# Performance work log

Measured on AMD Instinct MI355X. Metric: run time of the kernel, lower is better.

## Reference

```python
import jax, jax.numpy as jnp
import numpy as np

NUM_CODEBOOKS = 2
CODEBOOK_SIZE = 256
OUT_GROUP = 1
IN_GROUP = 8
IN_FEATURES = 4096
OUT_FEATURES = 11008


def setup_inputs() -> dict:
    key = jax.random.key(0)
    k1, k2, k3, k4, k5 = jax.random.split(key, 5)
    num_out_groups = OUT_FEATURES // OUT_GROUP
    num_in_groups = IN_FEATURES // IN_GROUP
    x = jax.random.normal(k1, (4, 2048, IN_FEATURES), dtype=jnp.float32)
    codes = jax.random.randint(k2, (num_out_groups, num_in_groups, NUM_CODEBOOKS), 0, CODEBOOK_SIZE, dtype=jnp.int32)
    codebooks = jax.random.normal(k3, (NUM_CODEBOOKS, CODEBOOK_SIZE, OUT_GROUP, IN_GROUP), dtype=jnp.float32) * 0.05
    scales = jax.random.uniform(k4, (num_out_groups, 1, 1, 1), dtype=jnp.float32)
    bias = jax.random.normal(k5, (OUT_FEATURES,), dtype=jnp.float32)
    return {"x": x, "codes": codes, "codebooks": codebooks, "scales": scales, "bias": bias}


def _dequantize_weight(codes, codebooks, scales):
    # codes: [Og, Ig, C] int; codebooks: [C, K, og, ig]; scales: [Og,1,1,1]
    C = codebooks.shape[0]
    og, ig = codebooks.shape[2], codebooks.shape[3]
    Og, Ig = codes.shape[0], codes.shape[1]
    # gather per-codebook vectors: result [Og, Ig, C, og, ig]
    w = codebooks[jnp.arange(C)[None, None, :], codes]
    w = w.sum(axis=2)                      # [Og, Ig, og, ig] (additive quantization)
    w = w * scales                         # broadcast [Og,1,1,1]
    w = w.transpose(0, 2, 1, 3)            # [Og, og, Ig, ig]
    return w.reshape(Og * og, Ig * ig)     # [out_features, in_features]


def reference(x, codes, codebooks, scales, bias):
    W = _dequantize_weight(codes, codebooks, scales)
    return jnp.einsum('bsi,oi->bso', x, W) + bias
```

## Files before the change

### kernel.cpp

```cpp
#include <hip/hip_runtime.h>
#include <hip/hip_bf16.h>
#include <stdint.h>

#define IN_F 4096
#define OUT_F 11008
#define M_ROWS 8192
#define NIG 512
#define CBSZ 256

typedef _Float16 f16x8 __attribute__((ext_vector_type(8)));
typedef float f32x4 __attribute__((ext_vector_type(4)));

__global__ __launch_bounds__(256) void dequant_w_kernel(
    const int* __restrict__ codes, const float* __restrict__ cbs,
    _Float16* __restrict__ W)
{
  const int idx = blockIdx.x * 256 + threadIdx.x;
  const int2 c = ((const int2*)codes)[idx];
  const float4* e0 = (const float4*)(cbs + (size_t)c.x * 8);
  const float4* e1 = (const float4*)(cbs + (size_t)CBSZ * 8 + (size_t)c.y * 8);
  const float4 a0 = e0[0], a1 = e0[1];
  const float4 b0 = e1[0], b1 = e1[1];
  f16x8 w;
  w[0] = (_Float16)(a0.x + b0.x);
  w[1] = (_Float16)(a0.y + b0.y);
  w[2] = (_Float16)(a0.z + b0.z);
  w[3] = (_Float16)(a0.w + b0.w);
  w[4] = (_Float16)(a1.x + b1.x);
  w[5] = (_Float16)(a1.y + b1.y);
  w[6] = (_Float16)(a1.z + b1.z);
  w[7] = (_Float16)(a1.w + b1.w);
  *(f16x8*)(W + (size_t)idx * 8) = w;
}

__global__ __launch_bounds__(256) void convert_x_kernel(
    const float* __restrict__ x, _Float16* __restrict__ X)
{
  const size_t i = ((size_t)blockIdx.x * 256 + threadIdx.x) * 8;
  const float4 a = *(const float4*)(x + i);
  const float4 b = *(const float4*)(x + i + 4);
  f16x8 v;
  v[0] = (_Float16)a.x; v[1] = (_Float16)a.y;
  v[2] = (_Float16)a.z; v[3] = (_Float16)a.w;
  v[4] = (_Float16)b.x; v[5] = (_Float16)b.y;
  v[6] = (_Float16)b.z; v[7] = (_Float16)b.w;
  *(f16x8*)(X + i) = v;
}

#define BM 256
#define BN 256
#define BK 64
#define NKT (IN_F / BK)
#define GRID_MT (M_ROWS / BM)
#define GRID_NT (OUT_F / BN)

__global__ __launch_bounds__(512, 2) void gemm_pipe(
    const _Float16* __restrict__ X, const _Float16* __restrict__ Wd,
    const float* __restrict__ scales, const float* __restrict__ bias,
    float* __restrict__ out)
{
  __shared__ char smem[131072];

  const int cpx = (GRID_MT * GRID_NT) >> 3;
  const int wg = (blockIdx.x & 7) * cpx + (blockIdx.x >> 3);
  const int mt = wg & (GRID_MT - 1), nt = wg >> 5;
  const int m0 = mt * BM, n0 = nt * BN;

  const int t = threadIdx.x;
  const int wave = t >> 6, lane = t & 63;
  const int wm = wave >> 2, wn = wave & 3;
  const int r16 = lane & 15;
  const int q = lane >> 4;
  const int sw = r16 & 7;
  const int c0 = ((q ^ sw) << 4);
  const int c1 = (((4 | q) ^ sw) << 4);

  const int s_row0 = t >> 3;
  const int s_col  = (((t & 7) ^ ((t >> 3) & 7)) << 3);
  const _Float16* asrc = X  + (size_t)(m0 + s_row0) * IN_F + s_col;
  const _Float16* bsrc = Wd + (size_t)(n0 + s_row0) * IN_F + s_col;
  const int s_dst = wave * 1024;

  f32x4 acc[8][4] = {};
  f16x8 alo[4][2], ahi[4][2], blo[2][2], bhi[2][2];

#define STAGE(kt, b) do {                                                     \
    const _Float16* _a = asrc + (size_t)(kt) * BK;                            \
    const _Float16* _b = bsrc + (size_t)(kt) * BK;                            \
    _Pragma("unroll")                                                         \
    for (int i = 0; i < 4; ++i)                                               \
      __builtin_amdgcn_global_load_lds(                                       \
        (const __attribute__((address_space(1))) void*)(_a + (size_t)i * 64 * IN_F), \
        (__attribute__((address_space(3))) void*)(smem + (b) * 65536 + i * 8192 + s_dst), \
        16, 0, 0);                                                            \
    _Pragma("unroll")                                                         \
    for (int i = 0; i < 4; ++i)                                               \
      __builtin_amdgcn_global_load_lds(                                       \
        (const __attribute__((address_space(1))) void*)(_b + (size_t)i * 64 * IN_F), \
        (__attribute__((address_space(3))) void*)(smem + (b) * 65536 + 32768 + i * 8192 + s_dst), \
        16, 0, 0);                                                            \
  } while (0)

#define BAR   __builtin_amdgcn_s_barrier()
#define PRIO1 __builtin_amdgcn_s_setprio(1)
#define PRIO0 __builtin_amdgcn_s_setprio(0)
#define VMCNT8 asm volatile("s_waitcnt vmcnt(8)" ::: "memory")
#define VMCNT0 asm volatile("s_waitcnt vmcnt(0)" ::: "memory")

#define QUAD(AM, BM_, AOFF, BOFF)                                             \
    _Pragma("unroll")                                                         \
    for (int k = 0; k < 2; ++k)                                               \
      _Pragma("unroll")                                                       \
      for (int m = 0; m < 4; ++m)                                             \
        _Pragma("unroll")                                                     \
        for (int n = 0; n < 2; ++n)                                           \
          acc[(AOFF) + m][(BOFF) + n] =                                       \
            __builtin_amdgcn_mfma_f32_16x16x32_f16(AM[m][k], BM_[n][k],       \
                                                   acc[(AOFF) + m][(BOFF) + n], 0, 0, 0)

#define TILE(cur, jj, STG, W8, W0) do {                                       \
    const char* Ab = smem + (cur) * 65536;                                    \
    const char* Bb = Ab + 32768;                                              \
                                               \
    _Pragma("unroll")                                                         \
    for (int m = 0; m < 4; ++m)                                               \
      _Pragma("unroll")                                                       \
      for (int k = 0; k < 2; ++k)                                             \
        alo[m][k] = *(const f16x8*)(Ab + ((wm * 128 + m * 16 + r16) << 7) + (k ? c1 : c0)); \
    _Pragma("unroll")                                                         \
    for (int n = 0; n < 2; ++n)                                               \
      _Pragma("unroll")                                                       \
      for (int k = 0; k < 2; ++k)                                             \
        blo[n][k] = *(const f16x8*)(Bb + ((wn * 64 + n * 16 + r16) << 7) + (k ? c1 : c0)); \
    BAR; PRIO1; QUAD(alo, blo, 0, 0); PRIO0; BAR;                             \
                                                      \
    _Pragma("unroll")                                                         \
    for (int n = 0; n < 2; ++n)                                               \
      _Pragma("unroll")                                                       \
      for (int k = 0; k < 2; ++k)                                             \
        bhi[n][k] = *(const f16x8*)(Bb + ((wn * 64 + (2 + n) * 16 + r16) << 7) + (k ? c1 : c0)); \
    BAR; PRIO1; QUAD(alo, bhi, 0, 2); PRIO0; BAR;                             \
                                                      \
    _Pragma("unroll")                                                         \
    for (int m = 0; m < 4; ++m)                                               \
      _Pragma("unroll")                                                       \
      for (int k = 0; k < 2; ++k)                                             \
        ahi[m][k] = *(const f16x8*)(Ab + ((wm * 128 + (4 + m) * 16 + r16) << 7) + (k ? c1 : c0)); \
    BAR; PRIO1; QUAD(ahi, bhi, 4, 2); PRIO0; BAR;                             \
     \
    if (STG) STAGE((jj) + 2, cur);                                            \
    BAR; PRIO1; QUAD(ahi, blo, 4, 0); PRIO0;                                  \
    if (W8) { VMCNT8; }                                                       \
    if (W0) { VMCNT0; }                                                       \
    if ((W8) || (W0)) BAR;                             \
  } while (0)

  STAGE(0, 0);
  STAGE(1, 1);
  VMCNT8;
  BAR;

  #pragma unroll 1
  for (int jj = 0; jj < 62; jj += 2) {
    TILE(0, jj, 1, 1, 0);
    TILE(1, jj + 1, 1, 1, 0);
  }
  TILE(0, 62, 0, 0, 1);
  TILE(1, 63, 0, 0, 0);

  const int crow = (lane >> 4) << 2;
  #pragma unroll
  for (int nf = 0; nf < 4; ++nf) {
    const int col = n0 + wn * 64 + nf * 16 + r16;
    const float s = scales[col];
    const float bb = bias[col];
    #pragma unroll
    for (int mf = 0; mf < 8; ++mf) {
      const int rb = m0 + wm * 128 + mf * 16 + crow;
      #pragma unroll
      for (int r = 0; r < 4; ++r)
        out[(size_t)(rb + r) * OUT_F + col] = acc[mf][nf][r] * s + bb;
    }
  }
#undef TILE
#undef QUAD
#undef STAGE
}

__global__ __launch_bounds__(256) void naive_kernel(
    const float* __restrict__ x, const int* __restrict__ codes,
    const float* __restrict__ cbs, const float* __restrict__ scales,
    const float* __restrict__ bias, float* __restrict__ out)
{
  __shared__ float xrow[IN_F];
  const int m = blockIdx.x;
  for (int i = threadIdx.x; i < IN_F; i += 256)
    xrow[i] = x[(size_t)m * IN_F + i];
  __syncthreads();
  for (int o = threadIdx.x; o < OUT_F; o += 256) {
    float acc = 0.f;
    const int2* crow = (const int2*)codes + (size_t)o * NIG;
    for (int g = 0; g < NIG; ++g) {
      const int2 c = crow[g];
      const float* e0 = cbs + (size_t)c.x * 8;
      const float* e1 = cbs + (size_t)CBSZ * 8 + (size_t)c.y * 8;
      const float* xr = xrow + g * 8;
      #pragma unroll
      for (int j = 0; j < 8; ++j) acc += (e0[j] + e1[j]) * xr[j];
    }
    out[(size_t)m * OUT_F + o] = acc * scales[o] + bias[o];
  }
}

extern "C" void kernel_launch(void* const* d_in, const int* in_sizes, int n_in,
                              void* d_out, int out_size, void* d_ws, size_t ws_size,
                              hipStream_t stream) {
  const float* x      = (const float*)d_in[0];
  const int*   codes  = (const int*)d_in[1];
  const float* cbs    = (const float*)d_in[2];
  const float* scales = (const float*)d_in[3];
  const float* bias   = (const float*)d_in[4];
  float* out = (float*)d_out;

  const size_t W_BYTES = (size_t)OUT_F * IN_F * sizeof(_Float16);
  const size_t X_BYTES = (size_t)M_ROWS * IN_F * sizeof(_Float16);

  if (ws_size < W_BYTES + X_BYTES) {
    naive_kernel<<<M_ROWS, 256, 0, stream>>>(x, codes, cbs, scales, bias, out);
    return;
  }

  _Float16* W = (_Float16*)d_ws;
  _Float16* X = (_Float16*)((char*)d_ws + W_BYTES);

  dequant_w_kernel<<<(OUT_F * NIG) / 256, 256, 0, stream>>>(codes, cbs, W);
  convert_x_kernel<<<(M_ROWS * IN_F / 8) / 256, 256, 0, stream>>>(x, X);
  gemm_pipe<<<GRID_MT * GRID_NT, 512, 0, stream>>>(X, W, scales, bias, out);
}
```

Baseline: 839.5 us.

## Restructure GEMM main loop into finer-grained interleaved LDS reads, MFMAs and staggered loads

Rewrites the GEMM tile loop so each K-tile is split into eight MFMA groups, with LDS fragment reads for the next group interleaved between them. Global-to-LDS loads are now issued in pairs spread across the tile, with A and B staged at different lookahead distances and finer vmcnt waits. Register fragments for the next tile are prefetched at the end of the current one. The aim is to hide LDS and global latency behind MFMA work. In exchange it adds more barriers, more live registers and more intricate buffer hazards.

```diff
diff --git a/kernel.cpp b/kernel.cpp
--- a/kernel.cpp
+++ b/kernel.cpp
@@ -66,8 +66,8 @@
   const int mt = wg & (GRID_MT - 1), nt = wg >> 5;
   const int m0 = mt * BM, n0 = nt * BN;
 
-  const int t = threadIdx.x;
-  const int wave = t >> 6, lane = t & 63;
+  const int t_ = threadIdx.x;
+  const int wave = t_ >> 6, lane = t_ & 63;
   const int wm = wave >> 2, wn = wave & 3;
   const int r16 = lane & 15;
   const int q = lane >> 4;
@@ -75,98 +75,113 @@
   const int c0 = ((q ^ sw) << 4);
   const int c1 = (((4 | q) ^ sw) << 4);
 
-  const int s_row0 = t >> 3;
-  const int s_col  = (((t & 7) ^ ((t >> 3) & 7)) << 3);
+  const int s_row0 = t_ >> 3;
+  const int s_col  = (((t_ & 7) ^ ((t_ >> 3) & 7)) << 3);
   const _Float16* asrc = X  + (size_t)(m0 + s_row0) * IN_F + s_col;
   const _Float16* bsrc = Wd + (size_t)(n0 + s_row0) * IN_F + s_col;
   const int s_dst = wave * 1024;
 
   f32x4 acc[8][4] = {};
-  f16x8 alo[4][2], ahi[4][2], blo[2][2], bhi[2][2];
-
-#define STAGE(kt, b) do {                                                     \
-    const _Float16* _a = asrc + (size_t)(kt) * BK;                            \
-    const _Float16* _b = bsrc + (size_t)(kt) * BK;                            \
-    _Pragma("unroll")                                                         \
-    for (int i = 0; i < 4; ++i)                                               \
-      __builtin_amdgcn_global_load_lds(                                       \
-        (const __attribute__((address_space(1))) void*)(_a + (size_t)i * 64 * IN_F), \
-        (__attribute__((address_space(3))) void*)(smem + (b) * 65536 + i * 8192 + s_dst), \
-        16, 0, 0);                                                            \
-    _Pragma("unroll")                                                         \
-    for (int i = 0; i < 4; ++i)                                               \
-      __builtin_amdgcn_global_load_lds(                                       \
-        (const __attribute__((address_space(1))) void*)(_b + (size_t)i * 64 * IN_F), \
-        (__attribute__((address_space(3))) void*)(smem + (b) * 65536 + 32768 + i * 8192 + s_dst), \
-        16, 0, 0);                                                            \
-  } while (0)
+  f16x8 al0[4], al1[4], ah0[4], ah1[4];
+  f16x8 bl0[2][2], bl1[2], bh0[2], bh1[2];
+
+#define GLD(gsrc, ldst) __builtin_amdgcn_global_load_lds(                     \
+    (const __attribute__((address_space(1))) void*)(gsrc),                    \
+    (__attribute__((address_space(3))) void*)(ldst), 16, 0, 0)
+#define STAGE_A(kt, bufc, i) GLD(asrc + (size_t)(kt) * BK + (size_t)(i) * 64 * IN_F, \
+    smem + (bufc) * 65536 + (i) * 8192 + s_dst)
+#define STAGE_B(kt, bufc, i) GLD(bsrc + (size_t)(kt) * BK + (size_t)(i) * 64 * IN_F, \
+    smem + (bufc) * 65536 + 32768 + (i) * 8192 + s_dst)
+
+#define RD_A(bufp, mm, cc) (*(const f16x8*)((bufp) + ((wm * 128 + (mm) * 16 + r16) << 7) + (cc)))
+#define RD_B(bufp, nn, cc) (*(const f16x8*)((bufp) + 32768 + ((wn * 64 + (nn) * 16 + r16) << 7) + (cc)))
 
 #define BAR   __builtin_amdgcn_s_barrier()
 #define PRIO1 __builtin_amdgcn_s_setprio(1)
 #define PRIO0 __builtin_amdgcn_s_setprio(0)
-#define VMCNT8 asm volatile("s_waitcnt vmcnt(8)" ::: "memory")
-#define VMCNT0 asm volatile("s_waitcnt vmcnt(0)" ::: "memory")
-
-#define QUAD(AM, BM_, AOFF, BOFF)                                             \
-    _Pragma("unroll")                                                         \
-    for (int k = 0; k < 2; ++k)                                               \
-      _Pragma("unroll")                                                       \
-      for (int m = 0; m < 4; ++m)                                             \
-        _Pragma("unroll")                                                     \
-        for (int n = 0; n < 2; ++n)                                           \
-          acc[(AOFF) + m][(BOFF) + n] =                                       \
-            __builtin_amdgcn_mfma_f32_16x16x32_f16(AM[m][k], BM_[n][k],       \
-                                                   acc[(AOFF) + m][(BOFF) + n], 0, 0, 0)
-
-#define TILE(cur, jj, STG, W8, W0) do {                                       \
-    const char* Ab = smem + (cur) * 65536;                                    \
-    const char* Bb = Ab + 32768;                                              \
-                                               \
+#define VM4 asm volatile("s_waitcnt vmcnt(4)" ::: "memory")
+#define VM2 asm volatile("s_waitcnt vmcnt(2)" ::: "memory")
+#define VM0 asm volatile("s_waitcnt vmcnt(0)" ::: "memory")
+
+#define MG(AF, BF, MO, NO)                                                    \
     _Pragma("unroll")                                                         \
     for (int m = 0; m < 4; ++m)                                               \
       _Pragma("unroll")                                                       \
-      for (int k = 0; k < 2; ++k)                                             \
-        alo[m][k] = *(const f16x8*)(Ab + ((wm * 128 + m * 16 + r16) << 7) + (k ? c1 : c0)); \
-    _Pragma("unroll")                                                         \
-    for (int n = 0; n < 2; ++n)                                               \
-      _Pragma("unroll")                                                       \
-      for (int k = 0; k < 2; ++k)                                             \
-        blo[n][k] = *(const f16x8*)(Bb + ((wn * 64 + n * 16 + r16) << 7) + (k ? c1 : c0)); \
-    BAR; PRIO1; QUAD(alo, blo, 0, 0); PRIO0; BAR;                             \
-                                                      \
-    _Pragma("unroll")                                                         \
-    for (int n = 0; n < 2; ++n)                                               \
-      _Pragma("unroll")                                                       \
-      for (int k = 0; k < 2; ++k)                                             \
-        bhi[n][k] = *(const f16x8*)(Bb + ((wn * 64 + (2 + n) * 16 + r16) << 7) + (k ? c1 : c0)); \
-    BAR; PRIO1; QUAD(alo, bhi, 0, 2); PRIO0; BAR;                             \
-                                                      \
-    _Pragma("unroll")                                                         \
-    for (int m = 0; m < 4; ++m)                                               \
-      _Pragma("unroll")                                                       \
-      for (int k = 0; k < 2; ++k)                                             \
-        ahi[m][k] = *(const f16x8*)(Ab + ((wm * 128 + (4 + m) * 16 + r16) << 7) + (k ? c1 : c0)); \
-    BAR; PRIO1; QUAD(ahi, bhi, 4, 2); PRIO0; BAR;                             \
-     \
-    if (STG) STAGE((jj) + 2, cur);                                            \
-    BAR; PRIO1; QUAD(ahi, blo, 4, 0); PRIO0;                                  \
-    if (W8) { VMCNT8; }                                                       \
-    if (W0) { VMCNT0; }                                                       \
-    if ((W8) || (W0)) BAR;                             \
+      for (int n = 0; n < 2; ++n)                                             \
+        acc[(MO) + m][(NO) + n] = __builtin_amdgcn_mfma_f32_16x16x32_f16(     \
+            AF[m], BF[n], acc[(MO) + m][(NO) + n], 0, 0, 0)
+
+#define TILE(P, tt, SA, SB, GB, GA) do {                                      \
+    char* bufT = smem + (P) * 65536;                                          \
+    char* bufN = smem + (1 - (P)) * 65536;                                    \
+                                                                      \
+    if (SA) { STAGE_A((tt) + 1, 1 - (P), 0); STAGE_A((tt) + 1, 1 - (P), 1); } \
+    _Pragma("unroll")                                                         \
+    for (int m = 0; m < 4; ++m) al1[m] = RD_A(bufT, m, c1);                   \
+    PRIO1; MG(al0, bl0[P], 0, 0); PRIO0; BAR;                                 \
+                                                                      \
+    if (SA) { STAGE_A((tt) + 1, 1 - (P), 2); STAGE_A((tt) + 1, 1 - (P), 3); } \
+    _Pragma("unroll")                                                         \
+    for (int n = 0; n < 2; ++n) bh1[n] = RD_B(bufT, 2 + n, c1);               \
+    PRIO1; MG(al1, bl1, 0, 0); PRIO0; BAR;                                    \
+                                                                      \
+    _Pragma("unroll")                                                         \
+    for (int n = 0; n < 2; ++n) bh0[n] = RD_B(bufT, 2 + n, c0);               \
+    PRIO1; MG(al1, bh1, 0, 2); PRIO0; BAR;                                    \
+                                                                      \
+    _Pragma("unroll")                                                         \
+    for (int m = 0; m < 4; ++m) ah0[m] = RD_A(bufT, 4 + m, c0);               \
+    PRIO1; MG(al0, bh0, 0, 2); PRIO0; BAR;                                    \
+                                                                      \
+    _Pragma("unroll")                                                         \
+    for (int m = 0; m < 4; ++m) ah1[m] = RD_A(bufT, 4 + m, c1);               \
+    PRIO1; MG(ah0, bh0, 4, 2); PRIO0; BAR;                                    \
+                                                                      \
+    PRIO1; MG(ah1, bh1, 4, 2); PRIO0;                                         \
+    if (GB) { VM4; }                                                          \
+    BAR;                                                                      \
+                                                                      \
+    if (SB) { STAGE_B((tt) + 2, P, 0); STAGE_B((tt) + 2, P, 1); }             \
+    _Pragma("unroll")                                                         \
+    for (int n = 0; n < 2; ++n) bl0[1 - (P)][n] = RD_B(bufN, n, c0);          \
+    PRIO1; MG(ah1, bl1, 4, 0); PRIO0;                                         \
+    if ((GA) == 2) { VM2; }                                                   \
+    if ((GA) == 0) { VM0; }                                                   \
+    BAR;                                                                      \
+                                                                      \
+    if (SB) { STAGE_B((tt) + 2, P, 2); STAGE_B((tt) + 2, P, 3); }             \
+    _Pragma("unroll")                                                         \
+    for (int m = 0; m < 4; ++m) al0[m] = RD_A(bufN, m, c0);                   \
+    _Pragma("unroll")                                                         \
+    for (int n = 0; n < 2; ++n) bl1[n] = RD_B(bufN, n, c1);                   \
+    PRIO1; MG(ah0, bl0[P], 4, 0); PRIO0; BAR;                                 \
   } while (0)
 
-  STAGE(0, 0);
-  STAGE(1, 1);
-  VMCNT8;
-  BAR;
+  {
+    _Pragma("unroll")
+    for (int i = 0; i < 4; ++i) { STAGE_A(0, 0, i); }
+    _Pragma("unroll")
+    for (int i = 0; i < 4; ++i) { STAGE_B(0, 0, i); }
+    _Pragma("unroll")
+    for (int i = 0; i < 4; ++i) { STAGE_B(1, 1, i); }
+    VM4;
+    BAR;
+    char* buf0p = smem;
+    _Pragma("unroll")
+    for (int n = 0; n < 2; ++n) bl0[0][n] = RD_B(buf0p, n, c0);
+    _Pragma("unroll")
+    for (int n = 0; n < 2; ++n) bl1[n] = RD_B(buf0p, n, c1);
+    _Pragma("unroll")
+    for (int m = 0; m < 4; ++m) al0[m] = RD_A(buf0p, m, c0);
+  }
 
   #pragma unroll 1
-  for (int jj = 0; jj < 62; jj += 2) {
-    TILE(0, jj, 1, 1, 0);
-    TILE(1, jj + 1, 1, 1, 0);
-  }
-  TILE(0, 62, 0, 0, 1);
-  TILE(1, 63, 0, 0, 0);
+  for (int t = 0; t < 62; t += 2) {
+    TILE(0, t,     1, 1, 1, 2);
+    TILE(1, t + 1, 1, 1, 1, 2);
+  }
+  TILE(0, 62, 1, 0, 1, 0);
+  TILE(1, 63, 0, 0, 0, -1);
 
   const int crow = (lane >> 4) << 2;
   #pragma unroll
@@ -183,8 +198,12 @@
     }
   }
 #undef TILE
-#undef QUAD
-#undef STAGE
+#undef MG
+#undef RD_A
+#undef RD_B
+#undef STAGE_A
+#undef STAGE_B
+#undef GLD
 }
 
 __global__ __launch_bounds__(256) void naive_kernel(
```

New measurement: 799.4 us. -4.8%, faster.
